# Kernel tuning notes

Hardware: AMD Instinct MI355X
Metric: run time of the kernel (lower is better)

The kernel has to match this reference:

```python
import jax, jax.numpy as jnp
import numpy as np

B, T, D, H = 64, 1024, 1, 256  # batch, seq_len, input_size(=output_size), hidden_size


def setup_inputs() -> dict:
    key = jax.random.key(0)
    ks = jax.random.split(key, 16)
    s = 1.0 / np.sqrt(H)  # torch LSTM/Linear default uniform init scale
    u = lambda k, shp: jax.random.uniform(k, shp, jnp.float32, -s, s)
    return {
        "x": jax.random.normal(ks[0], (B, T, D), jnp.float32),
        # encoder bidirectional 2-layer LSTM; leading dim 2 = (fwd, bwd); gate order i,f,g,o
        "enc_Wih_l0": u(ks[1], (2, 4 * H, D)),
        "enc_Whh_l0": u(ks[2], (2, 4 * H, H)),
        "enc_b_l0": u(ks[3], (2, 4 * H)),
        "enc_Wih_l1": u(ks[4], (2, 4 * H, 2 * H)),
        "enc_Whh_l1": u(ks[5], (2, 4 * H, H)),
        "enc_b_l1": u(ks[6], (2, 4 * H)),
        # decoder bidirectional 2-layer LSTM
        "dec_Wih_l0": u(ks[7], (2, 4 * H, D)),
        "dec_Whh_l0": u(ks[8], (2, 4 * H, H)),
        "dec_b_l0": u(ks[9], (2, 4 * H)),
        "dec_Wih_l1": u(ks[10], (2, 4 * H, 2 * H)),
        "dec_Whh_l1": u(ks[11], (2, 4 * H, H)),
        "dec_b_l1": u(ks[12], (2, 4 * H)),
        # output projection: Linear(2H -> 1)
        "fc_W": u(ks[13], (1, 2 * H)),
        "fc_b": u(ks[14], (1,)),
    }


def _cell(xt, h, c, Wih, Whh, b):
    # one LSTM cell step; xt: (B, Din), h/c: (B, H)
    gates = xt @ Wih.T + h @ Whh.T + b
    i, f, g, o = jnp.split(gates, 4, axis=-1)  # torch gate order i,f,g,o
    c = jax.nn.sigmoid(f) * c + jax.nn.sigmoid(i) * jnp.tanh(g)
    h = jax.nn.sigmoid(o) * jnp.tanh(c)
    return h, c


def _scan_dir(xs, Wih, Whh, b, reverse):
    # xs: (T, B, Din) time-major; returns (T,B,H) outputs aligned to input order + final (h,c)
    bsz = xs.shape[1]
    h0 = jnp.zeros((bsz, H), xs.dtype)
    def step(carry, xt):
        h, c = _cell(xt, carry[0], carry[1], Wih, Whh, b)
        return (h, c), h
    (hT, cT), ys = jax.lax.scan(step, (h0, h0), xs, reverse=reverse)
    return ys, hT, cT


def reference(x, enc_Wih_l0, enc_Whh_l0, enc_b_l0, enc_Wih_l1, enc_Whh_l1, enc_b_l1,
              dec_Wih_l0, dec_Whh_l0, dec_b_l0, dec_Wih_l1, dec_Whh_l1, dec_b_l1,
              fc_W, fc_b):
    xT = jnp.transpose(x, (1, 0, 2))  # (T, B, D)
    # ---- encoder: 2-layer bidirectional LSTM, zero initial state ----
    yf0, hf0, cf0 = _scan_dir(xT, enc_Wih_l0[0], enc_Whh_l0[0], enc_b_l0[0], False)
    yb0, hb0, cb0 = _scan_dir(xT, enc_Wih_l0[1], enc_Whh_l0[1], enc_b_l0[1], True)
    y0 = jnp.concatenate([yf0, yb0], axis=-1)  # (T, B, 2H)
    _, hf1, cf1 = _scan_dir(y0, enc_Wih_l1[0], enc_Whh_l1[0], enc_b_l1[0], False)
    _, hb1, cb1 = _scan_dir(y0, enc_Wih_l1[1], enc_Whh_l1[1], enc_b_l1[1], True)
    # torch state layout: [l0_fwd, l0_bwd, l1_fwd, l1_bwd]
    eh = (hf0, hb0, hf1, hb1)
    ec = (cf0, cb0, cf1, cb1)

    # ---- decoder: each step re-initializes LSTM state from ENCODER state (source bug,
    # reproduced faithfully); only the fc output feeds back as the next input ----
    def dec_step(x_in, _):
        hf, _c1 = _cell(x_in, eh[0], ec[0], dec_Wih_l0[0], dec_Whh_l0[0], dec_b_l0[0])
        hb, _c2 = _cell(x_in, eh[1], ec[1], dec_Wih_l0[1], dec_Whh_l0[1], dec_b_l0[1])
        z = jnp.concatenate([hf, hb], axis=-1)  # (B, 2H)
        hf1_, _c3 = _cell(z, eh[2], ec[2], dec_Wih_l1[0], dec_Whh_l1[0], dec_b_l1[0])
        hb1_, _c4 = _cell(z, eh[3], ec[3], dec_Wih_l1[1], dec_Whh_l1[1], dec_b_l1[1])
        y = jnp.concatenate([hf1_, hb1_], axis=-1) @ fc_W.T + fc_b  # (B, 1)
        return y, y

    x0 = jnp.zeros((x.shape[0], x.shape[2]), x.dtype)
    _, ys = jax.lax.scan(dec_step, x0, None, length=x.shape[1])  # (T, B, 1)
    return jnp.transpose(ys, (1, 0, 2))  # (B, T, 1)
```

## Files before the change

kernel.cpp:

```cpp
#include <hip/hip_runtime.h>
#include <hip/hip_bf16.h>
#include <hip/hip_fp16.h>
#include <math.h>


#define NWG 256
#define THR 512
#define U0S 132

#define ECL0   2048
#define EHL1   (ECL0 + 32768)
#define ECL1   (EHL1 + 16384)
#define ROF    (ECL1 + 32768)
#define WIH1T  (ROF + 262144)
#define GWR    (WIH1T + 524288)
#define PCF    (GWR + 1048576)
#define Y0OF   (PCF + 8192)
#define WS_REQ_BYTES ((size_t)(Y0OF + 16777216) * 4)

struct SeqParams {
  const void *x, *eWih0, *eWhh0, *eB0, *eWih1, *eWhh1, *eB1;
  const void *dWih0, *dWhh0, *dB0, *dWih1, *dWhh1, *dB1, *fcW, *fcb;
  void* out;
  float* ws;
  unsigned* ctrs;
};

typedef _Float16 hlf2 __attribute__((ext_vector_type(2)));
typedef _Float16 half8 __attribute__((ext_vector_type(8)));
typedef float floatx4 __attribute__((ext_vector_type(4)));

__device__ __forceinline__ float bf2f(unsigned short u) {
  return __uint_as_float(((unsigned)u) << 16);
}
__device__ __forceinline__ float hf2f(unsigned short u) {
  __half_raw r; r.x = u; return __half2float(__half(r));
}
__device__ __forceinline__ unsigned short f2h_u(float f) {
  __half h = __float2half(f);
  return *reinterpret_cast<unsigned short*>(&h);
}

__device__ __forceinline__ float fexp2(float x) {
#if __has_builtin(__builtin_amdgcn_exp2f)
  return __builtin_amdgcn_exp2f(x);
#else
  return exp2f(x);
#endif
}
__device__ __forceinline__ float frcp(float x) {
#if __has_builtin(__builtin_amdgcn_rcpf)
  return __builtin_amdgcn_rcpf(x);
#else
  return 1.0f / x;
#endif
}
__device__ __forceinline__ float sigm(float v) {
  return frcp(1.0f + fexp2(v * -1.44269504f));
}
__device__ __forceinline__ float ftanh(float v) {
  return fmaf(-2.0f, frcp(1.0f + fexp2(v * 2.88539008f)), 1.0f);
}

#if __has_builtin(__builtin_amdgcn_fdot2)
__device__ __forceinline__ float fdot2(hlf2 a, hlf2 b, float c) {
  return __builtin_amdgcn_fdot2(a, b, c, false);
}
#else
__device__ __forceinline__ float fdot2(hlf2 a, hlf2 b, float c) {
  return c + (float)a[0] * (float)b[0] + (float)a[1] * (float)b[1];
}
#endif

__device__ __forceinline__ float dot1(float a, const uint4& x, const uint4& y) {
  const hlf2* xp = reinterpret_cast<const hlf2*>(&x);
  const hlf2* yp = reinterpret_cast<const hlf2*>(&y);
  a = fdot2(xp[0], yp[0], a);
  a = fdot2(xp[1], yp[1], a);
  a = fdot2(xp[2], yp[2], a);
  a = fdot2(xp[3], yp[3], a);
  return a;
}
__device__ __forceinline__ void dot2acc(float4& a, const uint4& hv, const uint4& wv) {
  const hlf2* hp = reinterpret_cast<const hlf2*>(&hv);
  const hlf2* wp = reinterpret_cast<const hlf2*>(&wv);
  a.x = fdot2(hp[0], wp[0], a.x);
  a.y = fdot2(hp[1], wp[1], a.y);
  a.z = fdot2(hp[2], wp[2], a.z);
  a.w = fdot2(hp[3], wp[3], a.w);
}

__device__ __forceinline__ floatx4 mfma16(uint4 a, uint4 b, floatx4 c) {
  union { uint4 u; half8 h; } ua, ub;
  ua.u = a; ub.u = b;
  return __builtin_amdgcn_mfma_f32_16x16x32_f16(ua.h, ub.h, c, 0, 0, 0);
}

__device__ __forceinline__ float ldin(const void* p_, size_t i, int bf) {
  return bf ? bf2f(((const unsigned short*)p_)[i]) : ((const float*)p_)[i];
}
__device__ __forceinline__ void stout(void* o, size_t i, float v, int bf) {
  if (bf) ((__hip_bfloat16*)o)[i] = __float2bfloat16(v);
  else    ((float*)o)[i] = v;
}

__device__ __forceinline__ int detect_bf16(const void* xp) {
  const unsigned* u = (const unsigned*)xp;
  int votes = 0;
#pragma unroll 8
  for (int i = 0; i < 64; ++i) {
    unsigned e = (u[i] >> 7) & 0xFF;
    votes += (e >= 108 && e <= 131) ? 1 : 0;
  }
  return votes >= 32;
}

__device__ __forceinline__ void gbar(unsigned* ctrs, unsigned gen) {
  __syncthreads();
  if (threadIdx.x == 0) {
    __hip_atomic_fetch_add(&ctrs[(blockIdx.x & 31) * 32], 1u,
                           __ATOMIC_RELEASE, __HIP_MEMORY_SCOPE_AGENT);
  }
  if (threadIdx.x < 32) {
    while (__hip_atomic_load(&ctrs[threadIdx.x * 32], __ATOMIC_RELAXED,
                             __HIP_MEMORY_SCOPE_AGENT) < gen * 8u) {
      __builtin_amdgcn_s_sleep(1);
    }
    (void)__hip_atomic_load(&ctrs[threadIdx.x * 32], __ATOMIC_ACQUIRE,
                            __HIP_MEMORY_SCOPE_AGENT);
  }
  __syncthreads();
}

__device__ __forceinline__ uint4 ldw8(const void* src, size_t off, int bf) {
  union { __half h[8]; uint4 u; } r;
  if (bf) {
    const unsigned short* s = (const unsigned short*)src + off;
    ushort4 a = *reinterpret_cast<const ushort4*>(s);
    ushort4 b = *reinterpret_cast<const ushort4*>(s + 4);
    r.h[0] = __float2half(bf2f(a.x)); r.h[1] = __float2half(bf2f(a.y));
    r.h[2] = __float2half(bf2f(a.z)); r.h[3] = __float2half(bf2f(a.w));
    r.h[4] = __float2half(bf2f(b.x)); r.h[5] = __float2half(bf2f(b.y));
    r.h[6] = __float2half(bf2f(b.z)); r.h[7] = __float2half(bf2f(b.w));
  } else {
    const float* s = (const float*)src + off;
    float4 a = *reinterpret_cast<const float4*>(s);
    float4 b = *reinterpret_cast<const float4*>(s + 4);
    r.h[0] = __float2half(a.x); r.h[1] = __float2half(a.y);
    r.h[2] = __float2half(a.z); r.h[3] = __float2half(a.w);
    r.h[4] = __float2half(b.x); r.h[5] = __float2half(b.y);
    r.h[6] = __float2half(b.z); r.h[7] = __float2half(b.w);
  }
  return r.u;
}

__device__ __forceinline__ void stage_u128(unsigned* AH, const unsigned* src,
                                           int ustr, int uoff) {
  const int t = threadIdx.x;
#pragma unroll
  for (int i = 0; i < 4; ++i) {
    int idx = t + i * THR;
    int r = idx >> 5, c4 = (idx & 31) << 2;
    uint4 v = *reinterpret_cast<const uint4*>(src + (size_t)r * ustr + uoff + c4);
    *reinterpret_cast<uint4*>(AH + r * U0S + c4) = v;
  }
}
__device__ __forceinline__ void load_w16_rows(uint4 (&wr)[2][4], const void* src,
                                              int rowbase, int bf) {
  const int t = threadIdx.x, kc = t >> 6, rt = t & 3;
#pragma unroll
  for (int j = 0; j < 2; ++j) {
    size_t rb = (size_t)(rowbase + rt * 2 + j) * 256 + kc * 32;
#pragma unroll
    for (int d = 0; d < 4; ++d) wr[j][d] = ldw8(src, rb + d * 8, bf);
  }
}
__device__ __forceinline__ void dot2_t4(float4* acc, const unsigned* A,
                                        const uint4 (&wr)[2][4]) {
  const int t = threadIdx.x;
  const int kc = t >> 6, bt = (t & 63) >> 2;
#pragma unroll
  for (int d = 0; d < 4; ++d) {
    const int k = kc * 16 + d * 4;
    uint4 h0 = *reinterpret_cast<const uint4*>(A + (bt +  0) * U0S + k);
    uint4 h1 = *reinterpret_cast<const uint4*>(A + (bt + 16) * U0S + k);
    uint4 h2 = *reinterpret_cast<const uint4*>(A + (bt + 32) * U0S + k);
    uint4 h3 = *reinterpret_cast<const uint4*>(A + (bt + 48) * U0S + k);
    dot2acc(acc[0], h0, wr[0][d]); dot2acc(acc[1], h0, wr[1][d]);
    dot2acc(acc[2], h1, wr[0][d]); dot2acc(acc[3], h1, wr[1][d]);
    dot2acc(acc[4], h2, wr[0][d]); dot2acc(acc[5], h2, wr[1][d]);
    dot2acc(acc[6], h3, wr[0][d]); dot2acc(acc[7], h3, wr[1][d]);
  }
}
__device__ __forceinline__ void reduce_R(const float4* acc, float* part, float* dst,
                                         const void* bsrc, int rowbase, int bf) {
  const int t = threadIdx.x;
  const int kc = t >> 6, tile = t & 63;
#pragma unroll
  for (int e = 0; e < 8; ++e) {
    const float4 a = acc[e];
    part[e * 512 + kc * 64 + tile] = (a.x + a.y) + (a.z + a.w);
  }
  __syncthreads();
  {
    const int r = t >> 6, b = t & 63;
    const int tl = (b & 15) * 4 + (r >> 1);
    const float* pp = part + ((b >> 4) * 2 + (r & 1)) * 512 + tl;
    float v = ((pp[0] + pp[64]) + (pp[128] + pp[192])) +
              ((pp[256] + pp[320]) + (pp[384] + pp[448]));
    dst[(size_t)b * 1024 + rowbase + r] = v + ldin(bsrc, rowbase + r, bf);
  }
  __syncthreads();
}

__global__ void __launch_bounds__(THR, 2)
__attribute__((amdgpu_waves_per_eu(2, 2)))
seq2seq_kernel(SeqParams p) {
  __shared__ __align__(16) char smem[148736];
  uint4* FRAGu4 = (uint4*)smem;
  float* GF     = (float*)(smem + 131072);
  float* PREB   = (float*)(smem + 135168);
  float* PREWf  = (float*)(smem + 139264);
  float* XROW   = (float*)(smem + 143360);
  unsigned* H16 = (unsigned*)(smem + 147456);
  float* YL     = (float*)(smem + 148480);

  const int w = blockIdx.x;
  const int t = threadIdx.x;
  float* ws = p.ws;
  unsigned* ctrs = p.ctrs;
  unsigned* y0w   = (unsigned*)(ws + Y0OF);
  unsigned* EHL1u = (unsigned*)(ws + EHL1);
  uint4* WIH1Tu4  = (uint4*)(ws + WIH1T);
  unsigned* GWu   = (unsigned*)(ws + GWR);
  unsigned* flg   = (unsigned*)(ws + PCF);
  uint4* DWu4     = (uint4*)(ws + Y0OF);
  unsigned genF = 0;
  const int bfm = detect_bf16(p.x);
  const int enc_act = (w < 128);
  const int d = (w >> 6) & 1, b = w & 63;
  const int wv = t >> 6, l = t & 63;
  const int lg = l >> 4, lr = l & 15;

  uint4 awr[6][8];

  {
    if (w == 0) {
      for (int i = t; i < 8192; i += THR) flg[i] = 0u;
    }
    if (enc_act) {
      const void* whh0 = bfm ? (const void*)((const unsigned short*)p.eWhh0 + (size_t)d * 262144)
                             : (const void*)((const float*)p.eWhh0 + (size_t)d * 262144);
#pragma unroll
      for (int mt = 0; mt < 6; ++mt)
#pragma unroll
        for (int kc = 0; kc < 8; ++kc)
          awr[mt][kc] = ldw8(whh0,
              (size_t)(wv * 128 + mt * 16 + lr) * 256 + kc * 32 + lg * 8, bfm);
#pragma unroll
      for (int mt2 = 0; mt2 < 2; ++mt2)
#pragma unroll
        for (int kc = 0; kc < 8; ++kc)
          FRAGu4[(wv * 16 + mt2 * 8 + kc) * 64 + l] = ldw8(whh0,
              (size_t)(wv * 128 + (6 + mt2) * 16 + lr) * 256 + kc * 32 + lg * 8, bfm);
#pragma unroll
      for (int q = 0; q < 2; ++q) {
        PREB[t + q * 512]  = ldin(p.eB0,   d * 1024 + t + q * 512, bfm);
        PREWf[t + q * 512] = ldin(p.eWih0, d * 1024 + t + q * 512, bfm);
        XROW[t + q * 512]  = ldin(p.x, (size_t)b * 1024 + t + q * 512, bfm);
      }
      if (t < 256) H16[t] = 0u;
    } else {
#pragma unroll
      for (int q = 0; q < 2; ++q) {
        int idx = (w - 128) * 1024 + q * 512 + t;
        int dd = idx >> 16, rem = idx & 65535;
        int kc = rem >> 10, row = rem & 1023;
        WIH1Tu4[idx] = ldw8(p.eWih1, (size_t)dd * 524288 + (size_t)row * 512 + kc * 8, bfm);
      }
    }
  }
  gbar(ctrs, ++genF);

  if (enc_act) {
    float cc = 0.f;
    int pp = 0;
    unsigned ppw = 0;
    int ptt = -1;
    for (int st = 0; st < 1024; ++st) {
      const int tt = d ? (1023 - st) : st;
      if (ptt >= 0 && t < 256 && !(t & 1))
        y0w[(size_t)ptt * 16384 + (size_t)b * 256 + d * 128 + (t >> 1)] = ppw;
      float xv = (t < 256) ? XROW[tt] : 0.f;
      floatx4 acc[8];
#pragma unroll
      for (int m = 0; m < 8; ++m) acc[m] = (floatx4){0.f, 0.f, 0.f, 0.f};
      const uint4* hb4 = (const uint4*)(H16 + pp * 128);
#pragma unroll
      for (int kc = 0; kc < 8; ++kc) {
        uint4 bu = hb4[kc * 4 + lg];
        uint4 a6 = FRAGu4[(wv * 16 + kc) * 64 + l];
        uint4 a7 = FRAGu4[(wv * 16 + 8 + kc) * 64 + l];
        acc[0] = mfma16(awr[0][kc], bu, acc[0]);
        acc[1] = mfma16(awr[1][kc], bu, acc[1]);
        acc[2] = mfma16(awr[2][kc], bu, acc[2]);
        acc[3] = mfma16(awr[3][kc], bu, acc[3]);
        acc[4] = mfma16(awr[4][kc], bu, acc[4]);
        acc[5] = mfma16(awr[5][kc], bu, acc[5]);
        acc[6] = mfma16(a6, bu, acc[6]);
        acc[7] = mfma16(a7, bu, acc[7]);
      }
      if (lr == 0) {
#pragma unroll
        for (int m = 0; m < 8; ++m)
          *reinterpret_cast<floatx4*>(GF + wv * 128 + m * 16 + lg * 4) = acc[m];
      }
      __syncthreads();
      if (t < 256) {
        float gi = GF[t]       + PREB[t]       + xv * PREWf[t];
        float gf = GF[256 + t] + PREB[256 + t] + xv * PREWf[256 + t];
        float gg = GF[512 + t] + PREB[512 + t] + xv * PREWf[512 + t];
        float go = GF[768 + t] + PREB[768 + t] + xv * PREWf[768 + t];
        float cn = sigm(gf) * cc + sigm(gi) * ftanh(gg);
        float hn = sigm(go) * ftanh(cn);
        cc = cn;
        unsigned hu = (unsigned)f2h_u(hn);
        ((unsigned short*)(H16 + (pp ^ 1) * 128))[t] = (unsigned short)hu;
        unsigned nn = __shfl_down(hu, 1, 64);
        if (!(t & 1)) ppw = hu | (nn << 16);
        ptt = tt;
        if (st == 1023) ws[ECL0 + d * 16384 + b * 256 + t] = cn;
      }
      __syncthreads();
      pp ^= 1;
    }
    if (ptt >= 0 && t < 256 && !(t & 1))
      y0w[(size_t)ptt * 16384 + (size_t)b * 256 + d * 128 + (t >> 1)] = ppw;
  }
  gbar(ctrs, ++genF);

  {
    if (enc_act) {
      const void* whh1 = bfm ? (const void*)((const unsigned short*)p.eWhh1 + (size_t)d * 262144)
                             : (const void*)((const float*)p.eWhh1 + (size_t)d * 262144);
#pragma unroll
      for (int mt = 0; mt < 6; ++mt)
#pragma unroll
        for (int kc = 0; kc < 8; ++kc)
          awr[mt][kc] = ldw8(whh1,
              (size_t)(wv * 128 + mt * 16 + lr) * 256 + kc * 32 + lg * 8, bfm);
#pragma unroll
      for (int mt2 = 0; mt2 < 2; ++mt2)
#pragma unroll
        for (int kc = 0; kc < 8; ++kc)
          FRAGu4[(wv * 16 + mt2 * 8 + kc) * 64 + l] = ldw8(whh1,
              (size_t)(wv * 128 + (6 + mt2) * 16 + lr) * 256 + kc * 32 + lg * 8, bfm);
#pragma unroll
      for (int q = 0; q < 2; ++q)
        PREB[t + q * 512] = ldin(p.eB1, d * 1024 + t + q * 512, bfm);
      if (t < 256) H16[t] = 0u;
    }
  }
  gbar(ctrs, ++genF);

  if (enc_act) {
    float cc = 0.f;
    int pp = 0;
    for (int st = 0; st < 1024; ++st) {
      const int win = st >> 3, sl = st & 7;
      if (sl == 0) {
        if (t == 0) {
          while (__hip_atomic_load(&flg[w * 64], __ATOMIC_RELAXED,
                                   __HIP_MEMORY_SCOPE_AGENT) < (unsigned)(win + 1)) {
            __builtin_amdgcn_s_sleep(1);
          }
        }
        __atomic_signal_fence(__ATOMIC_ACQUIRE);
        __syncthreads();
      }
      unsigned gw0 = 0, gw1 = 0;
      if (t < 256) {
        const unsigned gb = (unsigned)w * 8192 + (unsigned)(win & 1) * 4096 + (unsigned)sl * 512;
        gw0 = __hip_atomic_load(&GWu[gb + t],       __ATOMIC_RELAXED, __HIP_MEMORY_SCOPE_AGENT);
        gw1 = __hip_atomic_load(&GWu[gb + 256 + t], __ATOMIC_RELAXED, __HIP_MEMORY_SCOPE_AGENT);
      }
      floatx4 acc[8];
#pragma unroll
      for (int m = 0; m < 8; ++m) acc[m] = (floatx4){0.f, 0.f, 0.f, 0.f};
      const uint4* hb4 = (const uint4*)(H16 + pp * 128);
#pragma unroll
      for (int kc = 0; kc < 8; ++kc) {
        uint4 bu = hb4[kc * 4 + lg];
        uint4 a6 = FRAGu4[(wv * 16 + kc) * 64 + l];
        uint4 a7 = FRAGu4[(wv * 16 + 8 + kc) * 64 + l];
        acc[0] = mfma16(awr[0][kc], bu, acc[0]);
        acc[1] = mfma16(awr[1][kc], bu, acc[1]);
        acc[2] = mfma16(awr[2][kc], bu, acc[2]);
        acc[3] = mfma16(awr[3][kc], bu, acc[3]);
        acc[4] = mfma16(awr[4][kc], bu, acc[4]);
        acc[5] = mfma16(awr[5][kc], bu, acc[5]);
        acc[6] = mfma16(a6, bu, acc[6]);
        acc[7] = mfma16(a7, bu, acc[7]);
      }
      if (lr == 0) {
#pragma unroll
        for (int m = 0; m < 8; ++m)
          *reinterpret_cast<floatx4*>(GF + wv * 128 + m * 16 + lg * 4) = acc[m];
      }
      __syncthreads();
      if (t < 256) {
        float gi = GF[t]       + PREB[t]       + hf2f((unsigned short)(gw0 & 0xffffu));
        float gf = GF[256 + t] + PREB[256 + t] + hf2f((unsigned short)(gw1 & 0xffffu));
        float gg = GF[512 + t] + PREB[512 + t] + hf2f((unsigned short)(gw0 >> 16));
        float go = GF[768 + t] + PREB[768 + t] + hf2f((unsigned short)(gw1 >> 16));
        float cn = sigm(gf) * cc + sigm(gi) * ftanh(gg);
        float hn = sigm(go) * ftanh(cn);
        cc = cn;
        unsigned hu = (unsigned)f2h_u(hn);
        ((unsigned short*)(H16 + (pp ^ 1) * 128))[t] = (unsigned short)hu;
        if (st == 1023) {
          unsigned nn = __shfl_down(hu, 1, 64);
          if (!(t & 1))
            EHL1u[d * 8192 + b * 128 + (t >> 1)] = hu | (nn << 16);
          ws[ECL1 + d * 16384 + b * 256 + t] = cn;
        }
      }
      __syncthreads();
      if (sl == 7 && t == 0)
        __hip_atomic_store(&flg[w * 64 + 32], (unsigned)(win + 1),
                           __ATOMIC_RELAXED, __HIP_MEMORY_SCOPE_AGENT);
      pp ^= 1;
    }
  } else {
    const int chain = w - 128, dp = chain >> 6, bp = chain & 63;
    const uint4* Wt = WIH1Tu4 + (size_t)dp * 65536;
    uint4* YWu4 = (uint4*)smem;
    for (int win = 0; win < 128; ++win) {
      if (win >= 2) {
        if (t == 0) {
          while (__hip_atomic_load(&flg[chain * 64 + 32], __ATOMIC_RELAXED,
                                   __HIP_MEMORY_SCOPE_AGENT) < (unsigned)(win - 1)) {
            __builtin_amdgcn_s_sleep(1);
          }
        }
        __syncthreads();
      }
      {
        int s = t >> 6, kcc = t & 63;
        int tw = dp ? (1023 - (win * 8 + s)) : (win * 8 + s);
        YWu4[s * 64 + kcc] =
            *(const uint4*)(y0w + (size_t)tw * 16384 + (size_t)bp * 256 + kcc * 4);
      }
      __syncthreads();
      float a0[8], a1[8];
#pragma unroll
      for (int s = 0; s < 8; ++s) { a0[s] = 0.f; a1[s] = 0.f; }
      for (int kc = 0; kc < 64; ++kc) {
        uint4 w0 = Wt[kc * 1024 + t];
        uint4 w1 = Wt[kc * 1024 + 512 + t];
#pragma unroll
        for (int s = 0; s < 8; ++s) {
          uint4 yv = YWu4[s * 64 + kc];
          a0[s] = dot1(a0[s], yv, w0);
          a1[s] = dot1(a1[s], yv, w1);
        }
      }
      const unsigned gb = (unsigned)chain * 8192 + (unsigned)(win & 1) * 4096;
#pragma unroll
      for (int s = 0; s < 8; ++s) {
        unsigned pw = (unsigned)f2h_u(a0[s]) | ((unsigned)f2h_u(a1[s]) << 16);
        __hip_atomic_store(&GWu[gb + s * 512 + t], pw,
                           __ATOMIC_RELAXED, __HIP_MEMORY_SCOPE_AGENT);
      }
      __syncthreads();
      if (t == 0)
        __hip_atomic_store(&flg[chain * 64], (unsigned)(win + 1),
                           __ATOMIC_RELAXED, __HIP_MEMORY_SCOPE_AGENT);
    }
  }
  gbar(ctrs, ++genF);

  {
    unsigned* AH0 = (unsigned*)smem;
    float* part = (float*)(smem + 33792);
    const int m = w >> 6, wl6 = w & 63;
    const void* whh;
    if (bfm) whh = (m < 2) ? (const void*)((const unsigned short*)p.dWhh0 + (size_t)m * 262144)
                           : (const void*)((const unsigned short*)p.dWhh1 + (size_t)(m - 2) * 262144);
    else     whh = (m < 2) ? (const void*)((const float*)p.dWhh0 + (size_t)m * 262144)
                           : (const void*)((const float*)p.dWhh1 + (size_t)(m - 2) * 262144);
    const void* bb;
    if (bfm) bb = (m < 2) ? (const void*)((const unsigned short*)p.dB0 + m * 1024)
                          : (const void*)((const unsigned short*)p.dB1 + (m - 2) * 1024);
    else     bb = (m < 2) ? (const void*)((const float*)p.dB0 + m * 1024)
                          : (const void*)((const float*)p.dB1 + (m - 2) * 1024);
    if (m == 0)      stage_u128(AH0, y0w + (size_t)1023 * 16384, 256, 0);
    else if (m == 1) stage_u128(AH0, y0w, 256, 128);
    else             stage_u128(AH0, EHL1u + (m - 2) * 8192, 128, 0);
    __syncthreads();
    float* dst = ws + ROF + m * 65536;
    for (int pass = 0; pass < 2; ++pass) {
      const int rowbase = wl6 * 16 + pass * 8;
      uint4 wrA[2][4];
      load_w16_rows(wrA, whh, rowbase, bfm);
      float4 acc[8];
#pragma unroll
      for (int e = 0; e < 8; ++e) acc[e] = make_float4(0.f, 0.f, 0.f, 0.f);
      dot2_t4(acc, AH0, wrA);
      reduce_R(acc, part, dst, bb, rowbase, bfm);
    }
  }
  gbar(ctrs, ++genF);

  {
    int idx = w * 512 + t;
    int dd = idx >> 16, rem = idx & 65535;
    int kc = rem >> 10, row = rem & 1023;
    DWu4[idx] = ldw8(p.dWih1, (size_t)dd * 524288 + (size_t)row * 512 + kc * 8, bfm);
  }
  float r1i = 0.f, r1f = 0.f, r1g = 0.f, r1o = 0.f, coldc = 0.f, fwc = 0.f, fcb = 0.f;
  {
    float* R0L  = (float*)smem;
    float* WI0L = (float*)(smem + 8192);
    float* C0L  = (float*)(smem + 16384);
    if (w < 64) {
      const int bq = w;
#pragma unroll
      for (int i = 0; i < 4; ++i) {
        int r = t + i * THR;
        int dz = r >> 10, rr = r & 1023;
        R0L[r]  = ws[ROF + dz * 65536 + (size_t)bq * 1024 + rr];
        WI0L[r] = ldin(p.dWih0, dz * 1024 + rr, bfm);
      }
      C0L[t >= 512 ? 0 : t] = ws[ECL0 + (t >> 8) * 16384 + (size_t)bq * 256 + (t & 255)];
      const int dd2 = t >> 8, col = t & 255;
      r1i = ws[ROF + (2 + dd2) * 65536 + (size_t)bq * 1024 +       col];
      r1f = ws[ROF + (2 + dd2) * 65536 + (size_t)bq * 1024 + 256 + col];
      r1g = ws[ROF + (2 + dd2) * 65536 + (size_t)bq * 1024 + 512 + col];
      r1o = ws[ROF + (2 + dd2) * 65536 + (size_t)bq * 1024 + 768 + col];
      coldc = ws[ECL1 + dd2 * 16384 + (size_t)bq * 256 + col];
      fwc = ldin(p.fcW, dd2 * 256 + col, bfm);
      fcb = ldin(p.fcb, 0, bfm);
    }
  }
  gbar(ctrs, ++genF);

  if (w < 64) {
    const int bq = w;
    float* R0L  = (float*)smem;
    float* WI0L = (float*)(smem + 8192);
    float* C0L  = (float*)(smem + 16384);
    unsigned* ZV = (unsigned*)(smem + 18432);
    const int dd2 = t >> 8, col = t & 255;
    const uint4* DWt = DWu4 + (size_t)dd2 * 65536;

    {
      float gi = R0L[dd2 * 1024 +       col];
      float gf = R0L[dd2 * 1024 + 256 + col];
      float gg = R0L[dd2 * 1024 + 512 + col];
      float go = R0L[dd2 * 1024 + 768 + col];
      float cold = C0L[dd2 * 256 + col];
      float cn = sigm(gf) * cold + sigm(gi) * ftanh(gg);
      float hz = sigm(go) * ftanh(cn);
      ((unsigned short*)ZV)[t] = f2h_u(hz);
    }
    __syncthreads();

    float yp1 = 3.0e38f, yp2 = -3.0e38f;
    for (int st = 0; st < 1024; ++st) {
      float ai = 0.f, af = 0.f, ag = 0.f, ao = 0.f;
      for (int kc = 0; kc < 64; ++kc) {
        uint4 zv = *(const uint4*)(ZV + kc * 4);
        uint4 w0 = DWt[kc * 1024 +       col];
        uint4 w1 = DWt[kc * 1024 + 256 + col];
        uint4 w2 = DWt[kc * 1024 + 512 + col];
        uint4 w3 = DWt[kc * 1024 + 768 + col];
        ai = dot1(ai, zv, w0);
        af = dot1(af, zv, w1);
        ag = dot1(ag, zv, w2);
        ao = dot1(ao, zv, w3);
      }
      float gi = ai + r1i, gf = af + r1f, gg = ag + r1g, go = ao + r1o;
      float cn = sigm(gf) * coldc + sigm(gi) * ftanh(gg);
      float h1 = sigm(go) * ftanh(cn);
      GF[t] = h1 * fwc;
      __syncthreads();
      if (t < 64) {
        const float* q = GF + t;
        GF[t] = ((q[0] + q[64]) + (q[128] + q[192])) +
                ((q[256] + q[320]) + (q[384] + q[448]));
      }
      __syncthreads();
      if (t == 0) {
        float yy = fcb;
        for (int i = 0; i < 64; ++i) yy += GF[i];
        YL[0] = yy;
      }
      __syncthreads();
      float ynew = YL[0];
      if (t == 0) stout(p.out, (size_t)bq * 1024 + st, ynew, bfm);
      if (ynew == yp1) {
        for (int t2 = st + 1 + t; t2 < 1024; t2 += THR)
          stout(p.out, (size_t)bq * 1024 + t2, ynew, bfm);
        break;
      }
      if (ynew == yp2) {
        for (int t2 = st + 1 + t; t2 < 1024; t2 += THR)
          stout(p.out, (size_t)bq * 1024 + t2, ((t2 - st) & 1) ? yp1 : ynew, bfm);
        break;
      }
      yp2 = yp1; yp1 = ynew;
      if (st < 1023) {
        __syncthreads();
        float gi2 = ynew * WI0L[dd2 * 1024 +       col] + R0L[dd2 * 1024 +       col];
        float gf2 = ynew * WI0L[dd2 * 1024 + 256 + col] + R0L[dd2 * 1024 + 256 + col];
        float gg2 = ynew * WI0L[dd2 * 1024 + 512 + col] + R0L[dd2 * 1024 + 512 + col];
        float go2 = ynew * WI0L[dd2 * 1024 + 768 + col] + R0L[dd2 * 1024 + 768 + col];
        float cold = C0L[dd2 * 256 + col];
        float cn2 = sigm(gf2) * cold + sigm(gi2) * ftanh(gg2);
        float hz = sigm(go2) * ftanh(cn2);
        ((unsigned short*)ZV)[t] = f2h_u(hz);
        __syncthreads();
      }
    }
  }
}

__global__ void fill_sig(unsigned short* out, int n, float val) {
  int i = blockIdx.x * 256 + threadIdx.x;
  __hip_bfloat16 b = __float2bfloat16(val);
  if (i < n) out[i] = *reinterpret_cast<unsigned short*>(&b);
}

extern "C" void kernel_launch(void* const* d_in, const int* in_sizes, int n_in,
                              void* d_out, int out_size, void* d_ws, size_t ws_size,
                              hipStream_t stream) {
  (void)in_sizes; (void)n_in;
  if (ws_size < WS_REQ_BYTES) {
    float sig = 2048.0f + (float)(ws_size >> 20);
    fill_sig<<<(out_size + 255) / 256, 256, 0, stream>>>(
        (unsigned short*)d_out, out_size, sig);
    return;
  }
  hipMemsetAsync(d_ws, 0, 8192, stream);

  SeqParams p;
  p.x     = d_in[0];
  p.eWih0 = d_in[1];
  p.eWhh0 = d_in[2];
  p.eB0   = d_in[3];
  p.eWih1 = d_in[4];
  p.eWhh1 = d_in[5];
  p.eB1   = d_in[6];
  p.dWih0 = d_in[7];
  p.dWhh0 = d_in[8];
  p.dB0   = d_in[9];
  p.dWih1 = d_in[10];
  p.dWhh1 = d_in[11];
  p.dB1   = d_in[12];
  p.fcW   = d_in[13];
  p.fcb   = d_in[14];
  p.out   = d_out;
  p.ws    = (float*)d_ws;
  p.ctrs  = (unsigned*)d_ws;

  seq2seq_kernel<<<dim3(NWG), dim3(THR), 0, stream>>>(p);
}
```

Before: 6.131 ms.

## Remap encoder gate rows so each wave computes full LSTM cells in registers

The recurrent weight rows are reassigned so that each wave's MFMA tiles hold all four gates (i,f,g,o) for the same 32 hidden units. The cell update can then run directly on the accumulators, without staging gates through shared memory and an extra barrier. This removes one __syncthreads and the GF round trip per timestep. In layer 1 the input-gate contributions are also prefetched one step ahead into a double-buffered LDS area, taking the global load off the critical path. The cost is that the elementwise math is now replicated across all 16 lr lanes, and the new GWL buffer reuses the PREWf shared-memory region.

```diff
diff --git a/kernel.cpp b/kernel.cpp
--- a/kernel.cpp
+++ b/kernel.cpp
@@ -221,6 +221,7 @@
   float* GF     = (float*)(smem + 131072);
   float* PREB   = (float*)(smem + 135168);
   float* PREWf  = (float*)(smem + 139264);
+  unsigned* GWL = (unsigned*)(smem + 139264);
   float* XROW   = (float*)(smem + 143360);
   unsigned* H16 = (unsigned*)(smem + 147456);
   float* YL     = (float*)(smem + 148480);
@@ -252,17 +253,19 @@
       const void* whh0 = bfm ? (const void*)((const unsigned short*)p.eWhh0 + (size_t)d * 262144)
                              : (const void*)((const float*)p.eWhh0 + (size_t)d * 262144);
 #pragma unroll
-      for (int mt = 0; mt < 6; ++mt)
+      for (int g = 0; g < 3; ++g)
+#pragma unroll
+        for (int hf = 0; hf < 2; ++hf)
+#pragma unroll
+          for (int kc = 0; kc < 8; ++kc)
+            awr[g * 2 + hf][kc] = ldw8(whh0,
+                (size_t)(g * 256 + wv * 32 + hf * 16 + lr) * 256 + kc * 32 + lg * 8, bfm);
+#pragma unroll
+      for (int hf = 0; hf < 2; ++hf)
 #pragma unroll
         for (int kc = 0; kc < 8; ++kc)
-          awr[mt][kc] = ldw8(whh0,
-              (size_t)(wv * 128 + mt * 16 + lr) * 256 + kc * 32 + lg * 8, bfm);
-#pragma unroll
-      for (int mt2 = 0; mt2 < 2; ++mt2)
-#pragma unroll
-        for (int kc = 0; kc < 8; ++kc)
-          FRAGu4[(wv * 16 + mt2 * 8 + kc) * 64 + l] = ldw8(whh0,
-              (size_t)(wv * 128 + (6 + mt2) * 16 + lr) * 256 + kc * 32 + lg * 8, bfm);
+          FRAGu4[(wv * 16 + hf * 8 + kc) * 64 + l] = ldw8(whh0,
+              (size_t)(768 + wv * 32 + hf * 16 + lr) * 256 + kc * 32 + lg * 8, bfm);
 #pragma unroll
       for (int q = 0; q < 2; ++q) {
         PREB[t + q * 512]  = ldin(p.eB0,   d * 1024 + t + q * 512, bfm);
@@ -283,15 +286,23 @@
   gbar(ctrs, ++genF);
 
   if (enc_act) {
-    float cc = 0.f;
+    float cc[2][4];
+#pragma unroll
+    for (int hf = 0; hf < 2; ++hf)
+#pragma unroll
+      for (int r = 0; r < 4; ++r) cc[hf][r] = 0.f;
     int pp = 0;
-    unsigned ppw = 0;
+    uint2 py[2]; py[0] = make_uint2(0, 0); py[1] = make_uint2(0, 0);
     int ptt = -1;
     for (int st = 0; st < 1024; ++st) {
       const int tt = d ? (1023 - st) : st;
-      if (ptt >= 0 && t < 256 && !(t & 1))
-        y0w[(size_t)ptt * 16384 + (size_t)b * 256 + d * 128 + (t >> 1)] = ppw;
-      float xv = (t < 256) ? XROW[tt] : 0.f;
+      if (ptt >= 0 && lr == 0) {
+#pragma unroll
+        for (int hf = 0; hf < 2; ++hf)
+          *reinterpret_cast<uint2*>(y0w + (size_t)ptt * 16384 + (size_t)b * 256 +
+                                    d * 128 + wv * 16 + hf * 8 + lg * 2) = py[hf];
+      }
+      float xv = XROW[tt];
       floatx4 acc[8];
 #pragma unroll
       for (int m = 0; m < 8; ++m) acc[m] = (floatx4){0.f, 0.f, 0.f, 0.f};
@@ -310,32 +321,56 @@
         acc[6] = mfma16(a6, bu, acc[6]);
         acc[7] = mfma16(a7, bu, acc[7]);
       }
-      if (lr == 0) {
-#pragma unroll
-        for (int m = 0; m < 8; ++m)
-          *reinterpret_cast<floatx4*>(GF + wv * 128 + m * 16 + lg * 4) = acc[m];
-      }
-      __syncthreads();
-      if (t < 256) {
-        float gi = GF[t]       + PREB[t]       + xv * PREWf[t];
-        float gf = GF[256 + t] + PREB[256 + t] + xv * PREWf[256 + t];
-        float gg = GF[512 + t] + PREB[512 + t] + xv * PREWf[512 + t];
-        float go = GF[768 + t] + PREB[768 + t] + xv * PREWf[768 + t];
-        float cn = sigm(gf) * cc + sigm(gi) * ftanh(gg);
-        float hn = sigm(go) * ftanh(cn);
-        cc = cn;
-        unsigned hu = (unsigned)f2h_u(hn);
-        ((unsigned short*)(H16 + (pp ^ 1) * 128))[t] = (unsigned short)hu;
-        unsigned nn = __shfl_down(hu, 1, 64);
-        if (!(t & 1)) ppw = hu | (nn << 16);
-        ptt = tt;
-        if (st == 1023) ws[ECL0 + d * 16384 + b * 256 + t] = cn;
-      }
+#pragma unroll
+      for (int hf = 0; hf < 2; ++hf) {
+        const int c0 = wv * 32 + hf * 16 + lg * 4;
+        float4 pbI = *reinterpret_cast<const float4*>(PREB + c0);
+        float4 pbF = *reinterpret_cast<const float4*>(PREB + 256 + c0);
+        float4 pbG = *reinterpret_cast<const float4*>(PREB + 512 + c0);
+        float4 pbO = *reinterpret_cast<const float4*>(PREB + 768 + c0);
+        float4 pwI = *reinterpret_cast<const float4*>(PREWf + c0);
+        float4 pwF = *reinterpret_cast<const float4*>(PREWf + 256 + c0);
+        float4 pwG = *reinterpret_cast<const float4*>(PREWf + 512 + c0);
+        float4 pwO = *reinterpret_cast<const float4*>(PREWf + 768 + c0);
+        const float* bI = &pbI.x; const float* bF = &pbF.x;
+        const float* bG = &pbG.x; const float* bO = &pbO.x;
+        const float* wI = &pwI.x; const float* wF = &pwF.x;
+        const float* wG = &pwG.x; const float* wO = &pwO.x;
+        unsigned short hu[4];
+#pragma unroll
+        for (int r = 0; r < 4; ++r) {
+          float gi = acc[0 + hf][r] + bI[r] + xv * wI[r];
+          float gf = acc[2 + hf][r] + bF[r] + xv * wF[r];
+          float gg = acc[4 + hf][r] + bG[r] + xv * wG[r];
+          float go = acc[6 + hf][r] + bO[r] + xv * wO[r];
+          float cn = sigm(gf) * cc[hf][r] + sigm(gi) * ftanh(gg);
+          float hn = sigm(go) * ftanh(cn);
+          cc[hf][r] = cn;
+          hu[r] = f2h_u(hn);
+        }
+        unsigned u0 = (unsigned)hu[0] | ((unsigned)hu[1] << 16);
+        unsigned u1 = (unsigned)hu[2] | ((unsigned)hu[3] << 16);
+        py[hf] = make_uint2(u0, u1);
+        if (lr == 0) {
+          *reinterpret_cast<uint2*>(H16 + (pp ^ 1) * 128 + wv * 16 + hf * 8 + lg * 2) =
+              make_uint2(u0, u1);
+          if (st == 1023) {
+            float4 cv; cv.x = cc[hf][0]; cv.y = cc[hf][1];
+            cv.z = cc[hf][2]; cv.w = cc[hf][3];
+            *reinterpret_cast<float4*>(ws + ECL0 + d * 16384 + b * 256 + c0) = cv;
+          }
+        }
+      }
+      ptt = tt;
       __syncthreads();
       pp ^= 1;
     }
-    if (ptt >= 0 && t < 256 && !(t & 1))
-      y0w[(size_t)ptt * 16384 + (size_t)b * 256 + d * 128 + (t >> 1)] = ppw;
+    if (lr == 0) {
+#pragma unroll
+      for (int hf = 0; hf < 2; ++hf)
+        *reinterpret_cast<uint2*>(y0w + (size_t)ptt * 16384 + (size_t)b * 256 +
+                                  d * 128 + wv * 16 + hf * 8 + lg * 2) = py[hf];
+    }
   }
   gbar(ctrs, ++genF);
 
@@ -344,17 +379,19 @@
       const void* whh1 = bfm ? (const void*)((const unsigned short*)p.eWhh1 + (size_t)d * 262144)
                              : (const void*)((const float*)p.eWhh1 + (size_t)d * 262144);
 #pragma unroll
-      for (int mt = 0; mt < 6; ++mt)
+      for (int g = 0; g < 3; ++g)
+#pragma unroll
+        for (int hf = 0; hf < 2; ++hf)
+#pragma unroll
+          for (int kc = 0; kc < 8; ++kc)
+            awr[g * 2 + hf][kc] = ldw8(whh1,
+                (size_t)(g * 256 + wv * 32 + hf * 16 + lr) * 256 + kc * 32 + lg * 8, bfm);
+#pragma unroll
+      for (int hf = 0; hf < 2; ++hf)
 #pragma unroll
         for (int kc = 0; kc < 8; ++kc)
-          awr[mt][kc] = ldw8(whh1,
-              (size_t)(wv * 128 + mt * 16 + lr) * 256 + kc * 32 + lg * 8, bfm);
-#pragma unroll
-      for (int mt2 = 0; mt2 < 2; ++mt2)
-#pragma unroll
-        for (int kc = 0; kc < 8; ++kc)
-          FRAGu4[(wv * 16 + mt2 * 8 + kc) * 64 + l] = ldw8(whh1,
-              (size_t)(wv * 128 + (6 + mt2) * 16 + lr) * 256 + kc * 32 + lg * 8, bfm);
+          FRAGu4[(wv * 16 + hf * 8 + kc) * 64 + l] = ldw8(whh1,
+              (size_t)(768 + wv * 32 + hf * 16 + lr) * 256 + kc * 32 + lg * 8, bfm);
 #pragma unroll
       for (int q = 0; q < 2; ++q)
         PREB[t + q * 512] = ldin(p.eB1, d * 1024 + t + q * 512, bfm);
@@ -364,25 +401,41 @@
   gbar(ctrs, ++genF);
 
   if (enc_act) {
-    float cc = 0.f;
-    int pp = 0;
+    float cc[2][4];
+#pragma unroll
+    for (int hf = 0; hf < 2; ++hf)
+#pragma unroll
+      for (int r = 0; r < 4; ++r) cc[hf][r] = 0.f;
+    int pp = 0, sel = 0;
+    if (t == 0) {
+      while (__hip_atomic_load(&flg[w * 64], __ATOMIC_RELAXED,
+                               __HIP_MEMORY_SCOPE_AGENT) < 1u) {
+        __builtin_amdgcn_s_sleep(1);
+      }
+    }
+    __atomic_signal_fence(__ATOMIC_ACQUIRE);
+    __syncthreads();
+    GWL[t] = __hip_atomic_load(&GWu[(unsigned)w * 8192 + t],
+                               __ATOMIC_RELAXED, __HIP_MEMORY_SCOPE_AGENT);
+    __syncthreads();
     for (int st = 0; st < 1024; ++st) {
       const int win = st >> 3, sl = st & 7;
-      if (sl == 0) {
-        if (t == 0) {
-          while (__hip_atomic_load(&flg[w * 64], __ATOMIC_RELAXED,
-                                   __HIP_MEMORY_SCOPE_AGENT) < (unsigned)(win + 1)) {
-            __builtin_amdgcn_s_sleep(1);
+      if (st < 1023) {
+        const int su = st + 1, wn = su >> 3;
+        if ((su & 7) == 0) {
+          if (t == 0) {
+            while (__hip_atomic_load(&flg[w * 64], __ATOMIC_RELAXED,
+                                     __HIP_MEMORY_SCOPE_AGENT) < (unsigned)(wn + 1)) {
+              __builtin_amdgcn_s_sleep(1);
+            }
           }
+          __atomic_signal_fence(__ATOMIC_ACQUIRE);
+          __syncthreads();
         }
-        __atomic_signal_fence(__ATOMIC_ACQUIRE);
-        __syncthreads();
-      }
-      unsigned gw0 = 0, gw1 = 0;
-      if (t < 256) {
-        const unsigned gb = (unsigned)w * 8192 + (unsigned)(win & 1) * 4096 + (unsigned)sl * 512;
-        gw0 = __hip_atomic_load(&GWu[gb + t],       __ATOMIC_RELAXED, __HIP_MEMORY_SCOPE_AGENT);
-        gw1 = __hip_atomic_load(&GWu[gb + 256 + t], __ATOMIC_RELAXED, __HIP_MEMORY_SCOPE_AGENT);
+        GWL[(sel ^ 1) * 512 + t] = __hip_atomic_load(
+            &GWu[(unsigned)w * 8192 + (unsigned)(wn & 1) * 4096 +
+                 (unsigned)(su & 7) * 512 + t],
+            __ATOMIC_RELAXED, __HIP_MEMORY_SCOPE_AGENT);
       }
       floatx4 acc[8];
 #pragma unroll
@@ -402,34 +455,49 @@
         acc[6] = mfma16(a6, bu, acc[6]);
         acc[7] = mfma16(a7, bu, acc[7]);
       }
-      if (lr == 0) {
-#pragma unroll
-        for (int m = 0; m < 8; ++m)
-          *reinterpret_cast<floatx4*>(GF + wv * 128 + m * 16 + lg * 4) = acc[m];
-      }
-      __syncthreads();
-      if (t < 256) {
-        float gi = GF[t]       + PREB[t]       + hf2f((unsigned short)(gw0 & 0xffffu));
-        float gf = GF[256 + t] + PREB[256 + t] + hf2f((unsigned short)(gw1 & 0xffffu));
-        float gg = GF[512 + t] + PREB[512 + t] + hf2f((unsigned short)(gw0 >> 16));
-        float go = GF[768 + t] + PREB[768 + t] + hf2f((unsigned short)(gw1 >> 16));
-        float cn = sigm(gf) * cc + sigm(gi) * ftanh(gg);
-        float hn = sigm(go) * ftanh(cn);
-        cc = cn;
-        unsigned hu = (unsigned)f2h_u(hn);
-        ((unsigned short*)(H16 + (pp ^ 1) * 128))[t] = (unsigned short)hu;
-        if (st == 1023) {
-          unsigned nn = __shfl_down(hu, 1, 64);
-          if (!(t & 1))
-            EHL1u[d * 8192 + b * 128 + (t >> 1)] = hu | (nn << 16);
-          ws[ECL1 + d * 16384 + b * 256 + t] = cn;
+#pragma unroll
+      for (int hf = 0; hf < 2; ++hf) {
+        const int c0 = wv * 32 + hf * 16 + lg * 4;
+        float4 pbI = *reinterpret_cast<const float4*>(PREB + c0);
+        float4 pbF = *reinterpret_cast<const float4*>(PREB + 256 + c0);
+        float4 pbG = *reinterpret_cast<const float4*>(PREB + 512 + c0);
+        float4 pbO = *reinterpret_cast<const float4*>(PREB + 768 + c0);
+        uint4 gA = *reinterpret_cast<const uint4*>(GWL + sel * 512 + c0);
+        uint4 gB = *reinterpret_cast<const uint4*>(GWL + sel * 512 + 256 + c0);
+        const float* bI = &pbI.x; const float* bF = &pbF.x;
+        const float* bG = &pbG.x; const float* bO = &pbO.x;
+        const unsigned* ga = &gA.x; const unsigned* gbp = &gB.x;
+        unsigned short hu[4];
+#pragma unroll
+        for (int r = 0; r < 4; ++r) {
+          float gi = acc[0 + hf][r] + bI[r] + hf2f((unsigned short)(ga[r] & 0xffffu));
+          float gf = acc[2 + hf][r] + bF[r] + hf2f((unsigned short)(gbp[r] & 0xffffu));
+          float gg = acc[4 + hf][r] + bG[r] + hf2f((unsigned short)(ga[r] >> 16));
+          float go = acc[6 + hf][r] + bO[r] + hf2f((unsigned short)(gbp[r] >> 16));
+          float cn = sigm(gf) * cc[hf][r] + sigm(gi) * ftanh(gg);
+          float hn = sigm(go) * ftanh(cn);
+          cc[hf][r] = cn;
+          hu[r] = f2h_u(hn);
+        }
+        unsigned u0 = (unsigned)hu[0] | ((unsigned)hu[1] << 16);
+        unsigned u1 = (unsigned)hu[2] | ((unsigned)hu[3] << 16);
+        if (lr == 0) {
+          *reinterpret_cast<uint2*>(H16 + (pp ^ 1) * 128 + wv * 16 + hf * 8 + lg * 2) =
+              make_uint2(u0, u1);
+          if (st == 1023) {
+            *reinterpret_cast<uint2*>(EHL1u + d * 8192 + b * 128 + wv * 16 + hf * 8 + lg * 2) =
+                make_uint2(u0, u1);
+            float4 cv; cv.x = cc[hf][0]; cv.y = cc[hf][1];
+            cv.z = cc[hf][2]; cv.w = cc[hf][3];
+            *reinterpret_cast<float4*>(ws + ECL1 + d * 16384 + b * 256 + c0) = cv;
+          }
         }
       }
       __syncthreads();
       if (sl == 7 && t == 0)
         __hip_atomic_store(&flg[w * 64 + 32], (unsigned)(win + 1),
                            __ATOMIC_RELAXED, __HIP_MEMORY_SCOPE_AGENT);
-      pp ^= 1;
+      pp ^= 1; sel ^= 1;
     }
   } else {
     const int chain = w - 128, dp = chain >> 6, bp = chain & 63;
```

Result: slower. 8.512 ms (+38.8%).
